# Performance work log

Measured on AMD Instinct MI355X. Metric: run time of the kernel, lower is better.

Reference implementation:

```python
import jax, jax.numpy as jnp
import numpy as np

VNUM = 50000
D = 256
NE = 1600000


def setup_inputs() -> dict:
    key = jax.random.key(0)
    ks = jax.random.split(key, 10)
    return {
        "vrepr": jax.random.normal(ks[0], (VNUM, D), dtype=jnp.float32) * 0.1,
        "sidx": jax.random.randint(ks[1], (NE,), 0, VNUM, dtype=jnp.int32),
        "tidx": jax.random.randint(ks[2], (NE,), 0, VNUM, dtype=jnp.int32),
        "esgn": jnp.where(jax.random.uniform(ks[3], (NE,)) < 0.5, -1.0, 1.0).astype(jnp.float32),
        "enorm": jax.random.uniform(ks[4], (NE,), dtype=jnp.float32),
        "loc_w": jax.random.normal(ks[5], (D, D), dtype=jnp.float32) / np.sqrt(D),
        "loc_b": jax.random.normal(ks[6], (D,), dtype=jnp.float32) * 0.01,
        "std_w": jax.random.normal(ks[7], (D, D), dtype=jnp.float32) / np.sqrt(D),
        "std_b": jax.random.normal(ks[8], (D,), dtype=jnp.float32) * 0.01,
        "eps": jax.random.normal(ks[9], (VNUM, D), dtype=jnp.float32),
    }


def reference(vrepr, sidx, tidx, esgn, enorm, loc_w, loc_b, std_w, std_b, eps):
    # GraphConv: gather source node features, weight by enorm*esgn, scatter-add to targets
    w = (enorm * esgn)[:, None]              # [E, 1]
    msg = vrepr[sidx] * w                    # [E, D]
    ptr = jax.ops.segment_sum(msg, tidx, num_segments=vrepr.shape[0])  # [V, D]
    # Linear heads (torch Linear: y = x @ W.T + b)
    loc = ptr @ loc_w.T + loc_b
    std = jax.nn.softplus(ptr @ std_w.T + std_b) + 1e-7
    # rsample: loc + std * eps
    vsample = loc + std * eps
    return loc, std, vsample
```

## Files before the change

kernel.cpp:

```cpp
#include <hip/hip_runtime.h>

#define D 256
#define BM 128

typedef __attribute__((ext_vector_type(8))) short s16x8;
typedef __attribute__((ext_vector_type(4))) float f32x4;

static __device__ __forceinline__ unsigned short f2b(float f) {
    unsigned u = __float_as_uint(f);
    unsigned r = (u + 0x7fffu + ((u >> 16) & 1u)) >> 16;
    return (unsigned short)r;
}
static __device__ __forceinline__ unsigned pack2(float a, float b) {
    return (unsigned)f2b(a) | ((unsigned)f2b(b) << 16);
}

__global__ void prep_w_kernel(const float* __restrict__ lw, const float* __restrict__ sw,
                              unsigned short* __restrict__ wT) {
    int i = blockIdx.x * 256 + threadIdx.x;
    float v = (i < D * D) ? lw[i] : sw[i - D * D];
    wT[i] = f2b(v);
}

__global__ void conv_v_kernel(const float* __restrict__ vr, unsigned short* __restrict__ vb, int n8) {
    int i = blockIdx.x * 256 + threadIdx.x;
    if (i < n8) {
        float4 f0 = ((const float4*)vr)[2 * i];
        float4 f1 = ((const float4*)vr)[2 * i + 1];
        uint4 o;
        o.x = pack2(f0.x, f0.y);
        o.y = pack2(f0.z, f0.w);
        o.z = pack2(f1.x, f1.y);
        o.w = pack2(f1.z, f1.w);
        ((uint4*)vb)[i] = o;
    }
}

__global__ void hist_kernel(const int* __restrict__ tidx, int* __restrict__ cnt,
                            int* __restrict__ rank, int E) {
    int e = blockIdx.x * blockDim.x + threadIdx.x;
    if (e < E) rank[e] = atomicAdd(&cnt[tidx[e]], 1);
}

__global__ void scan_kernel(const int* __restrict__ cnt, int* __restrict__ off, int V, int E) {
    __shared__ int sums[1024];
    int tid = threadIdx.x;
    int CH = (V + 1023) >> 10;
    int beg = tid * CH;
    int end = min(beg + CH, V);
    int s = 0;
    for (int i = beg; i < end; ++i) s += cnt[i];
    sums[tid] = s;
    __syncthreads();
    for (int ofs = 1; ofs < 1024; ofs <<= 1) {
        int v = (tid >= ofs) ? sums[tid - ofs] : 0;
        __syncthreads();
        sums[tid] += v;
        __syncthreads();
    }
    int run = (tid == 0) ? 0 : sums[tid - 1];
    for (int i = beg; i < end; ++i) {
        off[i] = run;
        run += cnt[i];
    }
    if (tid == 1023) off[V] = E;
}

__global__ void fill_kernel(const int* __restrict__ sidx, const int* __restrict__ tidx,
                            const float* __restrict__ esgn, const float* __restrict__ enorm,
                            const int* __restrict__ off, const int* __restrict__ rank,
                            int2* __restrict__ pk, int E) {
    int e = blockIdx.x * blockDim.x + threadIdx.x;
    if (e >= E) return;
    int idx = off[tidx[e]] + rank[e];
    float w = enorm[e] * esgn[e];
    pk[idx] = make_int2(sidx[e], __float_as_int(w));
}

__global__ __launch_bounds__(256) void accum_kernel(const unsigned short* __restrict__ vb,
                                                    const int2* __restrict__ pk,
                                                    const int* __restrict__ off,
                                                    unsigned short* __restrict__ ptrb, int V) {
    int gid = blockIdx.x * blockDim.x + threadIdx.x;
    int v = gid >> 6;
    if (v >= V) return;
    int lane = threadIdx.x & 63;
    int half = lane >> 5;
    int c = lane & 31;
    int beg = off[v], end = off[v + 1];
    const uint4* base = (const uint4*)vb;
    float acc[8];
#pragma unroll
    for (int j = 0; j < 8; ++j) acc[j] = 0.f;
    int i = beg + half;
    for (; i + 2 < end; i += 4) {
        int2 p0 = pk[i];
        int2 p1 = pk[i + 2];
        float w0 = __int_as_float(p0.y);
        float w1 = __int_as_float(p1.y);
        uint4 a = base[(size_t)p0.x * 32 + c];
        uint4 b = base[(size_t)p1.x * 32 + c];
        acc[0] = fmaf(__uint_as_float(a.x << 16), w0, acc[0]);
        acc[1] = fmaf(__uint_as_float(a.x & 0xffff0000u), w0, acc[1]);
        acc[2] = fmaf(__uint_as_float(a.y << 16), w0, acc[2]);
        acc[3] = fmaf(__uint_as_float(a.y & 0xffff0000u), w0, acc[3]);
        acc[4] = fmaf(__uint_as_float(a.z << 16), w0, acc[4]);
        acc[5] = fmaf(__uint_as_float(a.z & 0xffff0000u), w0, acc[5]);
        acc[6] = fmaf(__uint_as_float(a.w << 16), w0, acc[6]);
        acc[7] = fmaf(__uint_as_float(a.w & 0xffff0000u), w0, acc[7]);
        acc[0] = fmaf(__uint_as_float(b.x << 16), w1, acc[0]);
        acc[1] = fmaf(__uint_as_float(b.x & 0xffff0000u), w1, acc[1]);
        acc[2] = fmaf(__uint_as_float(b.y << 16), w1, acc[2]);
        acc[3] = fmaf(__uint_as_float(b.y & 0xffff0000u), w1, acc[3]);
        acc[4] = fmaf(__uint_as_float(b.z << 16), w1, acc[4]);
        acc[5] = fmaf(__uint_as_float(b.z & 0xffff0000u), w1, acc[5]);
        acc[6] = fmaf(__uint_as_float(b.w << 16), w1, acc[6]);
        acc[7] = fmaf(__uint_as_float(b.w & 0xffff0000u), w1, acc[7]);
    }
    if (i < end) {
        int2 p = pk[i];
        float w = __int_as_float(p.y);
        uint4 a = base[(size_t)p.x * 32 + c];
        acc[0] = fmaf(__uint_as_float(a.x << 16), w, acc[0]);
        acc[1] = fmaf(__uint_as_float(a.x & 0xffff0000u), w, acc[1]);
        acc[2] = fmaf(__uint_as_float(a.y << 16), w, acc[2]);
        acc[3] = fmaf(__uint_as_float(a.y & 0xffff0000u), w, acc[3]);
        acc[4] = fmaf(__uint_as_float(a.z << 16), w, acc[4]);
        acc[5] = fmaf(__uint_as_float(a.z & 0xffff0000u), w, acc[5]);
        acc[6] = fmaf(__uint_as_float(a.w << 16), w, acc[6]);
        acc[7] = fmaf(__uint_as_float(a.w & 0xffff0000u), w, acc[7]);
    }
#pragma unroll
    for (int j = 0; j < 8; ++j) acc[j] += __shfl_xor(acc[j], 32, 64);
    if (half == 0) {
        uint4 o;
        o.x = pack2(acc[0], acc[1]);
        o.y = pack2(acc[2], acc[3]);
        o.z = pack2(acc[4], acc[5]);
        o.w = pack2(acc[6], acc[7]);
        *(uint4*)(ptrb + (size_t)v * D + c * 8) = o;
    }
}

__global__ __launch_bounds__(256) void head_mfma_kernel(const unsigned short* __restrict__ ptrb,
                                                        const unsigned short* __restrict__ wT,
                                                        const float* __restrict__ lb,
                                                        const float* __restrict__ sb,
                                                        const float* __restrict__ eps,
                                                        float* __restrict__ out, int V) {
    __shared__ unsigned short lA[BM][72];
    __shared__ unsigned short lB[BM][72];
    int c0 = blockIdx.x * 64;
    int v0 = blockIdx.y * BM;
    int tid = threadIdx.x;
    int wave = tid >> 6, lane = tid & 63;
    int quad = lane >> 4, m16 = lane & 15;
    bool fullA = (v0 + BM <= V);

    int sc_m[4], sc_kc[4], sc_n[4];
#pragma unroll
    for (int it = 0; it < 4; ++it) {
        int cc = it * 256 + tid;
        int m = cc >> 3, kc = (cc & 7) * 8;
        sc_m[it] = m; sc_kc[it] = kc;
        sc_n[it] = (m < 64) ? (c0 + m) : (D + c0 + (m - 64));
    }

    uint4 ra[4], rb[4];
#pragma unroll
    for (int it = 0; it < 4; ++it) {
        int vv = v0 + sc_m[it];
        ra[it] = (fullA || vv < V) ? *(const uint4*)(ptrb + (size_t)vv * D + sc_kc[it])
                                   : make_uint4(0, 0, 0, 0);
        rb[it] = *(const uint4*)(wT + (size_t)sc_n[it] * D + sc_kc[it]);
    }

    f32x4 acc[2][8];
    f32x4 zero = {0.f, 0.f, 0.f, 0.f};
#pragma unroll
    for (int i = 0; i < 2; ++i)
#pragma unroll
        for (int j = 0; j < 8; ++j) acc[i][j] = zero;

    for (int k0i = 0; k0i < 4; ++k0i) {
        if (k0i) __syncthreads();
#pragma unroll
        for (int it = 0; it < 4; ++it) {
            *(uint4*)&lA[sc_m[it]][sc_kc[it]] = ra[it];
            *(uint4*)&lB[sc_m[it]][sc_kc[it]] = rb[it];
        }
        __syncthreads();
        if (k0i < 3) {
            int k0 = (k0i + 1) * 64;
#pragma unroll
            for (int it = 0; it < 4; ++it) {
                int vv = v0 + sc_m[it];
                ra[it] = (fullA || vv < V) ? *(const uint4*)(ptrb + (size_t)vv * D + k0 + sc_kc[it])
                                           : make_uint4(0, 0, 0, 0);
                rb[it] = *(const uint4*)(wT + (size_t)sc_n[it] * D + k0 + sc_kc[it]);
            }
        }
#pragma unroll
        for (int kk = 0; kk < 2; ++kk) {
            int kb = kk * 32 + quad * 8;
            s16x8 a0 = *(const s16x8*)&lA[wave * 32 + m16][kb];
            s16x8 a1 = *(const s16x8*)&lA[wave * 32 + 16 + m16][kb];
#pragma unroll
            for (int nt = 0; nt < 8; ++nt) {
                s16x8 b = *(const s16x8*)&lB[nt * 16 + m16][kb];
                acc[0][nt] = __builtin_amdgcn_mfma_f32_16x16x32_bf16(a0, b, acc[0][nt], 0, 0, 0);
                acc[1][nt] = __builtin_amdgcn_mfma_f32_16x16x32_bf16(a1, b, acc[1][nt], 0, 0, 0);
            }
        }
    }

    size_t VD = (size_t)V * D;
    float lbv[4], sbv[4];
#pragma unroll
    for (int nt = 0; nt < 4; ++nt) {
        int cc = c0 + nt * 16 + m16;
        lbv[nt] = lb[cc];
        sbv[nt] = sb[cc];
    }
    const float* epsb = eps + (size_t)v0 * D;
    float* outb = out + (size_t)v0 * D;
#pragma unroll
    for (int mt = 0; mt < 2; ++mt) {
#pragma unroll
        for (int nt = 0; nt < 4; ++nt) {
#pragma unroll
            for (int r = 0; r < 4; ++r) {
                int row = wave * 32 + mt * 16 + quad * 4 + r;
                if (fullA || v0 + row < V) {
                    int o = row * D + c0 + nt * 16 + m16;
                    float lo = acc[mt][nt][r] + lbv[nt];
                    float pre = acc[mt][nt + 4][r] + sbv[nt];
                    float sp = fmaxf(pre, 0.f) + __logf(1.f + __expf(-fabsf(pre)));
                    float st = sp + 1e-7f;
                    float ep = __builtin_nontemporal_load(&epsb[o]);
                    __builtin_nontemporal_store(lo, &outb[o]);
                    __builtin_nontemporal_store(st, &outb[VD + o]);
                    __builtin_nontemporal_store(fmaf(st, ep, lo), &outb[2 * VD + o]);
                }
            }
        }
    }
}

extern "C" void kernel_launch(void* const* d_in, const int* in_sizes, int n_in,
                              void* d_out, int out_size, void* d_ws, size_t ws_size,
                              hipStream_t stream) {
    const float* vrepr = (const float*)d_in[0];
    const int*   sidx  = (const int*)d_in[1];
    const int*   tidx  = (const int*)d_in[2];
    const float* esgn  = (const float*)d_in[3];
    const float* enorm = (const float*)d_in[4];
    const float* loc_w = (const float*)d_in[5];
    const float* loc_b = (const float*)d_in[6];
    const float* std_w = (const float*)d_in[7];
    const float* std_b = (const float*)d_in[8];
    const float* eps   = (const float*)d_in[9];
    float* out = (float*)d_out;

    int E = in_sizes[1];
    int V = in_sizes[0] / D;

    char* ws = (char*)d_ws;
    size_t o = 0;
    unsigned short* vb   = (unsigned short*)(ws + o); o += (size_t)V * D * 2;
    unsigned short* ptrb = (unsigned short*)(ws + o); o += (size_t)V * D * 2;
    unsigned short* wT   = (unsigned short*)(ws + o); o += (size_t)2 * D * D * 2;
    int* off  = (int*)(ws + o); o += ((size_t)V + 16) * sizeof(int);
    int* cnt  = (int*)(ws + o); o += ((size_t)V + 16) * sizeof(int);
    int* rank = (int*)(ws + o); o += (size_t)E * sizeof(int);
    o = (o + 15) & ~(size_t)15;
    int2* pk = (int2*)(ws + o); o += (size_t)E * sizeof(int2);

    hipMemsetAsync(cnt, 0, (size_t)V * sizeof(int), stream);
    prep_w_kernel<<<(2 * D * D) / 256, 256, 0, stream>>>(loc_w, std_w, wT);
    conv_v_kernel<<<(V * (D / 8) + 255) / 256, 256, 0, stream>>>(vrepr, vb, V * (D / 8));
    hist_kernel<<<(E + 255) / 256, 256, 0, stream>>>(tidx, cnt, rank, E);
    scan_kernel<<<1, 1024, 0, stream>>>(cnt, off, V, E);
    fill_kernel<<<(E + 255) / 256, 256, 0, stream>>>(sidx, tidx, esgn, enorm, off, rank, pk, E);
    accum_kernel<<<(V * 64 + 255) / 256, 256, 0, stream>>>(vb, pk, off, ptrb, V);
    dim3 hgrid(4, (V + BM - 1) / BM);
    head_mfma_kernel<<<hgrid, 256, 0, stream>>>(ptrb, wT, loc_b, std_b, eps, out, V);
}
```

Baseline: 635.8 us.

## Pre-swizzle operands into MFMA fragment layout and drop LDS from head GEMM

The weight-prep and accumulation kernels now write their bf16 outputs directly in the per-lane 16x16x32 MFMA fragment order. The head kernel can then load A and B fragments straight from global memory without LDS staging or barriers. Each wave now computes a 16-row tile across all 512 output columns (loc and std) and holds 32 accumulators. The cost is that every wave re-reads the full 256 KB weight matrix from cache, and register pressure is high.

```diff
diff --git a/kernel.cpp b/kernel.cpp
--- a/kernel.cpp
+++ b/kernel.cpp
@@ -1,7 +1,6 @@
 #include <hip/hip_runtime.h>
 
 #define D 256
-#define BM 128
 
 typedef __attribute__((ext_vector_type(8))) short s16x8;
 typedef __attribute__((ext_vector_type(4))) float f32x4;
@@ -16,10 +15,14 @@
 }
 
 __global__ void prep_w_kernel(const float* __restrict__ lw, const float* __restrict__ sw,
-                              unsigned short* __restrict__ wT) {
+                              unsigned short* __restrict__ wTf) {
     int i = blockIdx.x * 256 + threadIdx.x;
     float v = (i < D * D) ? lw[i] : sw[i - D * D];
-    wT[i] = f2b(v);
+    int n = i >> 8;
+    int k = i & 255;
+    int lane = (n & 15) | (((k >> 3) & 3) << 4);
+    int unit = ((n >> 4) << 9) + ((k >> 5) << 6) + lane;
+    wTf[unit * 8 + (k & 7)] = f2b(v);
 }
 
 __global__ void conv_v_kernel(const float* __restrict__ vr, unsigned short* __restrict__ vb, int n8) {
@@ -80,7 +83,7 @@
 __global__ __launch_bounds__(256) void accum_kernel(const unsigned short* __restrict__ vb,
                                                     const int2* __restrict__ pk,
                                                     const int* __restrict__ off,
-                                                    unsigned short* __restrict__ ptrb, int V) {
+                                                    unsigned short* __restrict__ ptrf, int V) {
     int gid = blockIdx.x * blockDim.x + threadIdx.x;
     int v = gid >> 6;
     if (v >= V) return;
@@ -138,110 +141,67 @@
         o.y = pack2(acc[2], acc[3]);
         o.z = pack2(acc[4], acc[5]);
         o.w = pack2(acc[6], acc[7]);
-        *(uint4*)(ptrb + (size_t)v * D + c * 8) = o;
-    }
-}
-
-__global__ __launch_bounds__(256) void head_mfma_kernel(const unsigned short* __restrict__ ptrb,
-                                                        const unsigned short* __restrict__ wT,
-                                                        const float* __restrict__ lb,
-                                                        const float* __restrict__ sb,
-                                                        const float* __restrict__ eps,
-                                                        float* __restrict__ out, int V) {
-    __shared__ unsigned short lA[BM][72];
-    __shared__ unsigned short lB[BM][72];
-    int c0 = blockIdx.x * 64;
-    int v0 = blockIdx.y * BM;
-    int tid = threadIdx.x;
-    int wave = tid >> 6, lane = tid & 63;
+        int fl = (v & 15) | ((c & 3) << 4);
+        int unit = ((v >> 4) << 9) + ((c >> 2) << 6) + fl;
+        ((uint4*)ptrf)[unit] = o;
+    }
+}
+
+__global__ __launch_bounds__(256, 2) void head_mfma_kernel(const unsigned short* __restrict__ ptrf,
+                                                           const unsigned short* __restrict__ wTf,
+                                                           const float* __restrict__ lb,
+                                                           const float* __restrict__ sb,
+                                                           const float* __restrict__ eps,
+                                                           float* __restrict__ out, int V) {
+    int wave = threadIdx.x >> 6, lane = threadIdx.x & 63;
+    int mt = blockIdx.x * 4 + wave;
+    int v0 = mt << 4;
+    if (v0 >= V) return;
+
+    const s16x8* Af = (const s16x8*)ptrf + ((size_t)mt << 9) + lane;
+    const s16x8* Bf = (const s16x8*)wTf + lane;
+
+    s16x8 a[8];
+#pragma unroll
+    for (int kt = 0; kt < 8; ++kt) a[kt] = Af[kt << 6];
+
+    f32x4 acc[32];
+    f32x4 zero = {0.f, 0.f, 0.f, 0.f};
+#pragma unroll
+    for (int nt = 0; nt < 32; ++nt) acc[nt] = zero;
+
+#pragma unroll
+    for (int kt = 0; kt < 8; ++kt) {
+#pragma unroll
+        for (int nt = 0; nt < 32; ++nt) {
+            s16x8 b = Bf[(nt << 9) + (kt << 6)];
+            acc[nt] = __builtin_amdgcn_mfma_f32_16x16x32_bf16(a[kt], b, acc[nt], 0, 0, 0);
+        }
+    }
+
     int quad = lane >> 4, m16 = lane & 15;
-    bool fullA = (v0 + BM <= V);
-
-    int sc_m[4], sc_kc[4], sc_n[4];
-#pragma unroll
-    for (int it = 0; it < 4; ++it) {
-        int cc = it * 256 + tid;
-        int m = cc >> 3, kc = (cc & 7) * 8;
-        sc_m[it] = m; sc_kc[it] = kc;
-        sc_n[it] = (m < 64) ? (c0 + m) : (D + c0 + (m - 64));
-    }
-
-    uint4 ra[4], rb[4];
-#pragma unroll
-    for (int it = 0; it < 4; ++it) {
-        int vv = v0 + sc_m[it];
-        ra[it] = (fullA || vv < V) ? *(const uint4*)(ptrb + (size_t)vv * D + sc_kc[it])
-                                   : make_uint4(0, 0, 0, 0);
-        rb[it] = *(const uint4*)(wT + (size_t)sc_n[it] * D + sc_kc[it]);
-    }
-
-    f32x4 acc[2][8];
-    f32x4 zero = {0.f, 0.f, 0.f, 0.f};
-#pragma unroll
-    for (int i = 0; i < 2; ++i)
-#pragma unroll
-        for (int j = 0; j < 8; ++j) acc[i][j] = zero;
-
-    for (int k0i = 0; k0i < 4; ++k0i) {
-        if (k0i) __syncthreads();
-#pragma unroll
-        for (int it = 0; it < 4; ++it) {
-            *(uint4*)&lA[sc_m[it]][sc_kc[it]] = ra[it];
-            *(uint4*)&lB[sc_m[it]][sc_kc[it]] = rb[it];
-        }
-        __syncthreads();
-        if (k0i < 3) {
-            int k0 = (k0i + 1) * 64;
-#pragma unroll
-            for (int it = 0; it < 4; ++it) {
-                int vv = v0 + sc_m[it];
-                ra[it] = (fullA || vv < V) ? *(const uint4*)(ptrb + (size_t)vv * D + k0 + sc_kc[it])
-                                           : make_uint4(0, 0, 0, 0);
-                rb[it] = *(const uint4*)(wT + (size_t)sc_n[it] * D + k0 + sc_kc[it]);
-            }
-        }
-#pragma unroll
-        for (int kk = 0; kk < 2; ++kk) {
-            int kb = kk * 32 + quad * 8;
-            s16x8 a0 = *(const s16x8*)&lA[wave * 32 + m16][kb];
-            s16x8 a1 = *(const s16x8*)&lA[wave * 32 + 16 + m16][kb];
-#pragma unroll
-            for (int nt = 0; nt < 8; ++nt) {
-                s16x8 b = *(const s16x8*)&lB[nt * 16 + m16][kb];
-                acc[0][nt] = __builtin_amdgcn_mfma_f32_16x16x32_bf16(a0, b, acc[0][nt], 0, 0, 0);
-                acc[1][nt] = __builtin_amdgcn_mfma_f32_16x16x32_bf16(a1, b, acc[1][nt], 0, 0, 0);
-            }
-        }
-    }
-
     size_t VD = (size_t)V * D;
-    float lbv[4], sbv[4];
-#pragma unroll
-    for (int nt = 0; nt < 4; ++nt) {
-        int cc = c0 + nt * 16 + m16;
-        lbv[nt] = lb[cc];
-        sbv[nt] = sb[cc];
-    }
+    bool full = (v0 + 16 <= V);
     const float* epsb = eps + (size_t)v0 * D;
     float* outb = out + (size_t)v0 * D;
 #pragma unroll
-    for (int mt = 0; mt < 2; ++mt) {
-#pragma unroll
-        for (int nt = 0; nt < 4; ++nt) {
-#pragma unroll
-            for (int r = 0; r < 4; ++r) {
-                int row = wave * 32 + mt * 16 + quad * 4 + r;
-                if (fullA || v0 + row < V) {
-                    int o = row * D + c0 + nt * 16 + m16;
-                    float lo = acc[mt][nt][r] + lbv[nt];
-                    float pre = acc[mt][nt + 4][r] + sbv[nt];
-                    float sp = fmaxf(pre, 0.f) + __logf(1.f + __expf(-fabsf(pre)));
-                    float st = sp + 1e-7f;
-                    float ep = __builtin_nontemporal_load(&epsb[o]);
-                    __builtin_nontemporal_store(lo, &outb[o]);
-                    __builtin_nontemporal_store(st, &outb[VD + o]);
-                    __builtin_nontemporal_store(fmaf(st, ep, lo), &outb[2 * VD + o]);
-                }
+    for (int nt = 0; nt < 16; ++nt) {
+        int col = (nt << 4) + m16;
+        float lbv = lb[col];
+        float sbv = sb[col];
+#pragma unroll
+        for (int r = 0; r < 4; ++r) {
+            int row = (quad << 2) + r;
+            if (full || v0 + row < V) {
+                int o = row * D + col;
+                float lo = acc[nt][r] + lbv;
+                float pre = acc[nt + 16][r] + sbv;
+                float sp = fmaxf(pre, 0.f) + __logf(1.f + __expf(-fabsf(pre)));
+                float st = sp + 1e-7f;
+                float ep = __builtin_nontemporal_load(&epsb[o]);
+                __builtin_nontemporal_store(lo, &outb[o]);
+                __builtin_nontemporal_store(st, &outb[VD + o]);
+                __builtin_nontemporal_store(fmaf(st, ep, lo), &outb[2 * VD + o]);
             }
         }
     }
@@ -268,8 +228,8 @@
     char* ws = (char*)d_ws;
     size_t o = 0;
     unsigned short* vb   = (unsigned short*)(ws + o); o += (size_t)V * D * 2;
-    unsigned short* ptrb = (unsigned short*)(ws + o); o += (size_t)V * D * 2;
-    unsigned short* wT   = (unsigned short*)(ws + o); o += (size_t)2 * D * D * 2;
+    unsigned short* ptrf = (unsigned short*)(ws + o); o += (size_t)V * D * 2;
+    unsigned short* wTf  = (unsigned short*)(ws + o); o += (size_t)2 * D * D * 2;
     int* off  = (int*)(ws + o); o += ((size_t)V + 16) * sizeof(int);
     int* cnt  = (int*)(ws + o); o += ((size_t)V + 16) * sizeof(int);
     int* rank = (int*)(ws + o); o += (size_t)E * sizeof(int);
@@ -277,12 +237,11 @@
     int2* pk = (int2*)(ws + o); o += (size_t)E * sizeof(int2);
 
     hipMemsetAsync(cnt, 0, (size_t)V * sizeof(int), stream);
-    prep_w_kernel<<<(2 * D * D) / 256, 256, 0, stream>>>(loc_w, std_w, wT);
+    prep_w_kernel<<<(2 * D * D) / 256, 256, 0, stream>>>(loc_w, std_w, wTf);
     conv_v_kernel<<<(V * (D / 8) + 255) / 256, 256, 0, stream>>>(vrepr, vb, V * (D / 8));
     hist_kernel<<<(E + 255) / 256, 256, 0, stream>>>(tidx, cnt, rank, E);
     scan_kernel<<<1, 1024, 0, stream>>>(cnt, off, V, E);
     fill_kernel<<<(E + 255) / 256, 256, 0, stream>>>(sidx, tidx, esgn, enorm, off, rank, pk, E);
-    accum_kernel<<<(V * 64 + 255) / 256, 256, 0, stream>>>(vb, pk, off, ptrb, V);
-    dim3 hgrid(4, (V + BM - 1) / BM);
-    head_mfma_kernel<<<hgrid, 256, 0, stream>>>(ptrb, wT, loc_b, std_b, eps, out, V);
-}
+    accum_kernel<<<(V * 64 + 255) / 256, 256, 0, stream>>>(vb, pk, off, ptrf, V);
+    head_mfma_kernel<<<(V + 63) / 64, 256, 0, stream>>>(ptrf, wTf, loc_b, std_b, eps, out, V);
+}
```

New measurement: 697.7 us. +9.7%, slower.
